# Kernel optimization log

Measured on AMD Instinct MI355X. Metric: run time of the kernel, lower is better.

Reference implementation:

```python
import jax, jax.numpy as jnp
import numpy as np

B, N, G = 4096, 20, 4
D_IN, D_OUT, H = 128, 64, 8
LRELU = 0.2  # TF leaky_relu default alpha


def _glorot(key, shape):
    fan_in, fan_out = shape[-2], shape[-1]
    scale = jnp.sqrt(6.0 / (fan_in + fan_out)).astype(jnp.float32)
    return jax.random.uniform(key, shape, jnp.float32, -1.0, 1.0) * scale


def setup_inputs() -> dict:
    key = jax.random.key(0)
    k1, k2, k3, k4, k5, k6 = jax.random.split(key, 6)
    return {
        "self_vecs": jax.random.normal(k1, (B, G, D_IN), jnp.float32),
        "neigh_vecs": jax.random.normal(k2, (B, N, G, D_IN), jnp.float32),
        "W_heads": _glorot(k3, (H, D_IN, D_OUT)),      # per-head before_attend_weights
        "a_self": _glorot(k4, (H, D_OUT, 1))[..., 0],  # per-head attend_weights_self  [H, D_OUT]
        "a_neigh": _glorot(k5, (H, D_OUT, 1))[..., 0], # per-head attend_weights_neigh [H, D_OUT]
        "W_out": _glorot(k6, (H * D_OUT, D_OUT)),      # final FC weights
    }


def reference(self_vecs, neigh_vecs, W_heads, a_self, a_neigh, W_out):
    # Transform self and neighbor vectors for all heads at once.
    self_t = jnp.einsum("bgd,hde->bghe", self_vecs, W_heads)    # [B,G,H,E]
    neigh_t = jnp.einsum("bngd,hde->bnghe", neigh_vecs, W_heads)  # [B,N,G,H,E]

    f_self = jnp.einsum("bghe,he->bgh", self_t, a_self)          # [B,G,H]
    f_neigh = jnp.einsum("bnghe,he->bngh", neigh_t, a_neigh)     # [B,N,G,H]

    # logits [B,N,G,H]; original applies softmax over the num_graphs axis (tf default last axis of [B,N,G])
    logits = f_self[:, None, :, :] + f_neigh
    attend = jax.nn.softmax(jax.nn.leaky_relu(logits, LRELU), axis=2)  # softmax over G

    # Weighted aggregation over neighbors: [B,G,H,E]
    out_h = jnp.einsum("bngh,bnghe->bghe", attend, neigh_t)
    out_h = jax.nn.leaky_relu(out_h, LRELU)  # per-head activation (act=leaky_relu)

    # Concatenate heads along feature dim -> [B,G,H*E], final FC + relu
    h = out_h.reshape(out_h.shape[0], out_h.shape[1], H * D_OUT)
    return jax.nn.relu(jnp.einsum("bgk,ke->bge", h, W_out))
```

## Files before the change

kernel.cpp:

```cpp
#include <hip/hip_runtime.h>
#include <hip/hip_bf16.h>

#define BB 4096
#define NNB 20
#define GG 4
#define DIN 128
#define EE 64
#define HH 8

typedef short bf16x8 __attribute__((ext_vector_type(8)));
typedef float f32x4 __attribute__((ext_vector_type(4)));

__device__ __forceinline__ float lrelu_f(float x) { return x > 0.f ? x : 0.2f * x; }
__device__ __forceinline__ unsigned short f2bf(float f) {
  unsigned u = __float_as_uint(f);
  return (unsigned short)((u + 0x7fffu + ((u >> 16) & 1u)) >> 16);
}
__device__ __forceinline__ float bf2f(unsigned short s) {
  return __uint_as_float(((unsigned)s) << 16);
}

__global__ __launch_bounds__(256) void prep_kernel(
    const float* __restrict__ W_heads, const float* __restrict__ a_self,
    const float* __restrict__ a_neigh, const float* __restrict__ W_out,
    unsigned short* __restrict__ P1Whi, unsigned short* __restrict__ P1Wlo,
    unsigned short* __restrict__ WBhi, unsigned short* __restrict__ WBlo,
    unsigned short* __restrict__ WOhi, unsigned short* __restrict__ WOlo) {
  int id = blockIdx.x * 256 + threadIdx.x;
  if (id < 2048) {
    int j = id & 7, lane = (id >> 3) & 63, kb = id >> 9;
    int col = lane & 15, k = kb * 32 + (lane >> 4) * 8 + j;
    int h = col & 7;
    const float* a = (col < 8) ? a_neigh : a_self;
    const float* Wrow = W_heads + (h * DIN + k) * EE;
    float acc = 0.f;
    for (int e = 0; e < EE; ++e) acc = fmaf(Wrow[e], a[h * EE + e], acc);
    unsigned short hi = f2bf(acc);
    P1Whi[id] = hi;
    P1Wlo[id] = f2bf(acc - bf2f(hi));
  } else if (id < 2048 + 65536) {
    int rel = id - 2048;
    int j = rel & 7, l = (rel >> 3) & 63, kb = (rel >> 9) & 3, nt = (rel >> 11) & 3, h = rel >> 13;
    int d = kb * 32 + (l >> 4) * 8 + j;
    int e = nt * 16 + (l & 15);
    float w = W_heads[(h * DIN + d) * EE + e];
    unsigned short hi = f2bf(w);
    WBhi[rel] = hi;
    WBlo[rel] = f2bf(w - bf2f(hi));
  } else if (id < 2048 + 65536 + 32768) {
    int rel = id - 2048 - 65536;
    int j = rel & 7, l = (rel >> 3) & 63, kb = (rel >> 9) & 15, nt = rel >> 13;
    int k = kb * 32 + (l >> 4) * 8 + j;
    int n = nt * 16 + (l & 15);
    float w = W_out[k * EE + n];
    unsigned short hi = f2bf(w);
    WOhi[rel] = hi;
    WOlo[rel] = f2bf(w - bf2f(hi));
  }
}

__global__ __launch_bounds__(512, 4) void fused_kernel(
    const float* __restrict__ self_vecs, const float* __restrict__ neigh_vecs,
    const unsigned short* __restrict__ P1Whi, const unsigned short* __restrict__ P1Wlo,
    const unsigned short* __restrict__ WBhi, const unsigned short* __restrict__ WBlo,
    const unsigned short* __restrict__ WOhi, const unsigned short* __restrict__ WOlo,
    float* __restrict__ out) {
  __shared__ char smem[57344];
  char* aggb = smem;
  float* attw = (float*)(smem + 32768);
  char* hb = smem + 32768;

  const int t = threadIdx.x;
  const int w = t >> 6, lane = t & 63;
  const int m = lane & 15, kg = lane >> 4;
  const int bid = blockIdx.x;

#define LOAD_X(X, ptr)                                                         \
  {                                                                            \
    const float4* p_ = (const float4*)(ptr);                                   \
    _Pragma("unroll") for (int q = 0; q < 4; ++q) {                            \
      X[2 * q]     = p_[q * 8 + kg * 2];                                       \
      X[2 * q + 1] = p_[q * 8 + kg * 2 + 1];                                   \
    }                                                                          \
  }

#define PROC_TILE(X, cvec)                                                     \
  {                                                                            \
    _Pragma("unroll") for (int kb = 0; kb < 4; ++kb) {                         \
      float xv[8] = {X[2 * kb].x,     X[2 * kb].y,     X[2 * kb].z,            \
                     X[2 * kb].w,     X[2 * kb + 1].x, X[2 * kb + 1].y,        \
                     X[2 * kb + 1].z, X[2 * kb + 1].w};                        \
      bf16x8 xh;                                                               \
      _Pragma("unroll") for (int j = 0; j < 8; ++j) xh[j] = (short)f2bf(xv[j]); \
      bf16x8 wh = *(const bf16x8*)(smem + kb * 1024 + lane * 16);              \
      bf16x8 wl = *(const bf16x8*)(smem + 4096 + kb * 1024 + lane * 16);       \
      cvec = __builtin_amdgcn_mfma_f32_16x16x32_bf16(xh, wh, cvec, 0, 0, 0);   \
      cvec = __builtin_amdgcn_mfma_f32_16x16x32_bf16(xh, wl, cvec, 0, 0, 0);   \
    }                                                                          \
  }

#define P1_SOFTMAX(tile, cvec)                                                 \
  if (m < 8) {                                                                 \
    float l[4], mx = -1e30f;                                                   \
    _Pragma("unroll") for (int gg = 0; gg < 4; ++gg) {                         \
      float v = lrelu_f(fs[gg] + (cvec)[gg]);                                  \
      l[gg] = v;                                                               \
      mx = fmaxf(mx, v);                                                       \
    }                                                                          \
    float s = 0.f;                                                             \
    _Pragma("unroll") for (int gg = 0; gg < 4; ++gg) {                         \
      l[gg] = __expf(l[gg] - mx);                                              \
      s += l[gg];                                                              \
    }                                                                          \
    float inv = 1.f / s;                                                       \
    _Pragma("unroll") for (int gg = 0; gg < 4; ++gg)                           \
      attw[(tile) * 128 + (kg * 4 + gg) * 8 + m] = l[gg] * inv;                \
  }

  const int bl_m = m >> 2, g_m = m & 3;
  const float* base_n =
      neigh_vecs + ((size_t)(bid * 4 + bl_m) * NNB * GG + g_m) * DIN;

  float4 XS[8], XA[8], XB[8], XC[8];
  LOAD_X(XS, self_vecs + ((size_t)bid * 16 + m) * DIN)
  LOAD_X(XA, base_n + (size_t)w * (GG * DIN))

  {
    const float4* src = (t < 256) ? (const float4*)P1Whi : (const float4*)P1Wlo;
    ((float4*)smem)[t] = src[t & 255];
  }
  __syncthreads();

  f32x4 fs;
  {
    f32x4 c20 = {0.f, 0.f, 0.f, 0.f};
    PROC_TILE(XS, c20)
#pragma unroll
    for (int reg = 0; reg < 4; ++reg) fs[reg] = __shfl_xor(c20[reg], 8);
  }
  LOAD_X(XB, base_n + (size_t)(w + 8) * (GG * DIN))

  f32x4 cA = {0.f, 0.f, 0.f, 0.f}, cB = {0.f, 0.f, 0.f, 0.f};
  PROC_TILE(XA, cA)
  if (w < 4) LOAD_X(XC, base_n + (size_t)(w + 16) * (GG * DIN))
  PROC_TILE(XB, cB)
  if (w < 4) {
    f32x4 cC = {0.f, 0.f, 0.f, 0.f};
    PROC_TILE(XC, cC)
    P1_SOFTMAX(w + 16, cC)
  }
  P1_SOFTMAX(w, cA)
  P1_SOFTMAX(w + 8, cB)
  __syncthreads();

  {
    const int ih = lane >> 5;
    const int bg = 2 * w + ih;
    const int bl = w >> 1;
    const int g0 = (2 * w) & 3;
    const float* nb2 =
        neigh_vecs + ((size_t)(bid * 4 + bl) * NNB * GG + g0) * DIN;
    const int dl = 4 * (lane & 31);
    float acc[8][4];
#pragma unroll
    for (int h = 0; h < 8; ++h)
#pragma unroll
      for (int d = 0; d < 4; ++d) acc[h][d] = 0.f;
#pragma unroll
    for (int n = 0; n < NNB; ++n) {
      float4 x4 = *(const float4*)&nb2[(size_t)n * GG * DIN + 4 * lane];
      f32x4 a0 = *(const f32x4*)&attw[n * 128 + bg * 8];
      f32x4 a1 = *(const f32x4*)&attw[n * 128 + bg * 8 + 4];
#pragma unroll
      for (int h = 0; h < 4; ++h) {
        acc[h][0] = fmaf(a0[h], x4.x, acc[h][0]);
        acc[h][1] = fmaf(a0[h], x4.y, acc[h][1]);
        acc[h][2] = fmaf(a0[h], x4.z, acc[h][2]);
        acc[h][3] = fmaf(a0[h], x4.w, acc[h][3]);
        acc[h + 4][0] = fmaf(a1[h], x4.x, acc[h + 4][0]);
        acc[h + 4][1] = fmaf(a1[h], x4.y, acc[h + 4][1]);
        acc[h + 4][2] = fmaf(a1[h], x4.z, acc[h + 4][2]);
        acc[h + 4][3] = fmaf(a1[h], x4.w, acc[h + 4][3]);
      }
    }
    const int swz = (bg & 7) << 4;
#pragma unroll
    for (int h = 0; h < 8; ++h) {
      uint2 pk;
      pk.x = (unsigned)f2bf(acc[h][0]) | ((unsigned)f2bf(acc[h][1]) << 16);
      pk.y = (unsigned)f2bf(acc[h][2]) | ((unsigned)f2bf(acc[h][3]) << 16);
      *(uint2*)(aggb + ((bg * 2048 + h * 256 + 2 * dl) ^ swz)) = pk;
    }
  }
  __syncthreads();

  {
    const int hh = w;
    const int aswz = (m & 7) << 4;
    bf16x8 a[4];
#pragma unroll
    for (int kb = 0; kb < 4; ++kb)
      a[kb] = *(const bf16x8*)(aggb + ((m * 2048 + hh * 256 + kb * 64 + kg * 16) ^ aswz));
#pragma unroll
    for (int nt = 0; nt < 4; ++nt) {
      f32x4 c = {0.f, 0.f, 0.f, 0.f};
#pragma unroll
      for (int kb = 0; kb < 4; ++kb) {
        const int fi = (((hh * 4 + nt) * 4 + kb) * 64 + lane) * 8;
        bf16x8 bh = *(const bf16x8*)(WBhi + fi);
        bf16x8 bl_ = *(const bf16x8*)(WBlo + fi);
        c = __builtin_amdgcn_mfma_f32_16x16x32_bf16(a[kb], bh, c, 0, 0, 0);
        c = __builtin_amdgcn_mfma_f32_16x16x32_bf16(a[kb], bl_, c, 0, 0, 0);
      }
      const int k = hh * 64 + nt * 16 + m;
#pragma unroll
      for (int reg = 0; reg < 4; ++reg) {
        int row = kg * 4 + reg;
        int byte = (row * 1024 + k * 2) ^ ((row & 7) << 4);
        *(unsigned short*)(hb + byte) = f2bf(lrelu_f(c[reg]));
      }
    }
  }
  __syncthreads();

  if (w < 4) {
    const int nt = w;
    f32x4 acc = {0.f, 0.f, 0.f, 0.f};
    for (int kb = 0; kb < 16; ++kb) {
      int byte = (m * 1024 + (kb * 32 + kg * 8) * 2) ^ ((m & 7) << 4);
      bf16x8 ah = *(const bf16x8*)(hb + byte);
      const int fi = ((nt * 16 + kb) * 64 + lane) * 8;
      bf16x8 bh = *(const bf16x8*)(WOhi + fi);
      bf16x8 bl_ = *(const bf16x8*)(WOlo + fi);
      acc = __builtin_amdgcn_mfma_f32_16x16x32_bf16(ah, bh, acc, 0, 0, 0);
      acc = __builtin_amdgcn_mfma_f32_16x16x32_bf16(ah, bl_, acc, 0, 0, 0);
    }
    const int rbase = bid * 16;
#pragma unroll
    for (int reg = 0; reg < 4; ++reg) {
      int row = rbase + kg * 4 + reg;
      out[(size_t)row * EE + nt * 16 + m] = fmaxf(acc[reg], 0.f);
    }
  }
#undef LOAD_X
#undef PROC_TILE
#undef P1_SOFTMAX
}

extern "C" void kernel_launch(void* const* d_in, const int* in_sizes, int n_in,
                              void* d_out, int out_size, void* d_ws, size_t ws_size,
                              hipStream_t stream) {
  (void)in_sizes; (void)n_in; (void)out_size; (void)ws_size;
  const float* self_vecs  = (const float*)d_in[0];
  const float* neigh_vecs = (const float*)d_in[1];
  const float* W_heads    = (const float*)d_in[2];
  const float* a_self     = (const float*)d_in[3];
  const float* a_neigh    = (const float*)d_in[4];
  const float* W_out      = (const float*)d_in[5];
  float* out              = (float*)d_out;

  char* ws = (char*)d_ws;
  unsigned short* P1Whi = (unsigned short*)ws;
  unsigned short* P1Wlo = (unsigned short*)(ws + 4096);
  unsigned short* WBhi  = (unsigned short*)(ws + 8192);
  unsigned short* WBlo  = (unsigned short*)(ws + 8192 + 131072);
  unsigned short* WOhi  = (unsigned short*)(ws + 8192 + 262144);
  unsigned short* WOlo  = (unsigned short*)(ws + 8192 + 262144 + 65536);

  prep_kernel<<<(2048 + 65536 + 32768) / 256, 256, 0, stream>>>(
      W_heads, a_self, a_neigh, W_out, P1Whi, P1Wlo, WBhi, WBlo, WOhi, WOlo);

  fused_kernel<<<BB / 4, 512, 0, stream>>>(
      self_vecs, neigh_vecs, P1Whi, P1Wlo, WBhi, WBlo, WOhi, WOlo, out);
}
```

Before: 68.07 us.

## Halve work per block: 2 batches per 256-thread block, 2048 blocks

Restructures the fused kernel so each block handles 2 batch items (8 rows) with 4 waves instead of 4 items with 8 waves, doubling the grid and cutting shared memory to 24KB. Phase-1 tiles are processed in a five-stage software pipeline with prefetching, and phases 2-3 loop over two heads per wave. MFMA tiles now run half-empty (rows duplicated via m&7), which wastes matrix throughput. In exchange the change aims for more blocks and better occupancy and latency hiding on the memory-bound neighbor reads.

```diff
diff --git a/kernel.cpp b/kernel.cpp
--- a/kernel.cpp
+++ b/kernel.cpp
@@ -59,20 +59,21 @@
   }
 }
 
-__global__ __launch_bounds__(512, 4) void fused_kernel(
+__global__ __launch_bounds__(256, 4) void fused_kernel(
     const float* __restrict__ self_vecs, const float* __restrict__ neigh_vecs,
     const unsigned short* __restrict__ P1Whi, const unsigned short* __restrict__ P1Wlo,
     const unsigned short* __restrict__ WBhi, const unsigned short* __restrict__ WBlo,
     const unsigned short* __restrict__ WOhi, const unsigned short* __restrict__ WOlo,
     float* __restrict__ out) {
-  __shared__ char smem[57344];
+  __shared__ char smem[24576];
   char* aggb = smem;
-  float* attw = (float*)(smem + 32768);
-  char* hb = smem + 32768;
+  float* attw = (float*)(smem + 16384);
+  char* hb = smem + 16384;
 
   const int t = threadIdx.x;
   const int w = t >> 6, lane = t & 63;
   const int m = lane & 15, kg = lane >> 4;
+  const int m8 = m & 7;
   const int bid = blockIdx.x;
 
 #define LOAD_X(X, ptr)                                                         \
@@ -100,7 +101,7 @@
   }
 
 #define P1_SOFTMAX(tile, cvec)                                                 \
-  if (m < 8) {                                                                 \
+  if (m < 8 && kg < 2) {                                                       \
     float l[4], mx = -1e30f;                                                   \
     _Pragma("unroll") for (int gg = 0; gg < 4; ++gg) {                         \
       float v = lrelu_f(fs[gg] + (cvec)[gg]);                                  \
@@ -114,21 +115,19 @@
     }                                                                          \
     float inv = 1.f / s;                                                       \
     _Pragma("unroll") for (int gg = 0; gg < 4; ++gg)                           \
-      attw[(tile) * 128 + (kg * 4 + gg) * 8 + m] = l[gg] * inv;                \
-  }
-
-  const int bl_m = m >> 2, g_m = m & 3;
+      attw[(tile) * 64 + (kg * 4 + gg) * 8 + m] = l[gg] * inv;                 \
+  }
+
+  const int bl8 = m8 >> 2, g8 = m8 & 3;
   const float* base_n =
-      neigh_vecs + ((size_t)(bid * 4 + bl_m) * NNB * GG + g_m) * DIN;
-
-  float4 XS[8], XA[8], XB[8], XC[8];
-  LOAD_X(XS, self_vecs + ((size_t)bid * 16 + m) * DIN)
+      neigh_vecs + (((size_t)(bid * 2 + bl8) * NNB) * GG + g8) * DIN;
+
+  float4 XS[8], XA[8], XB[8], XC[8], XD[8], XE[8];
+  LOAD_X(XS, self_vecs + ((size_t)bid * 8 + m8) * DIN)
   LOAD_X(XA, base_n + (size_t)w * (GG * DIN))
 
-  {
-    const float4* src = (t < 256) ? (const float4*)P1Whi : (const float4*)P1Wlo;
-    ((float4*)smem)[t] = src[t & 255];
-  }
+  ((float4*)smem)[t]       = ((const float4*)P1Whi)[t];
+  ((float4*)smem)[256 + t] = ((const float4*)P1Wlo)[t];
   __syncthreads();
 
   f32x4 fs;
@@ -138,28 +137,44 @@
 #pragma unroll
     for (int reg = 0; reg < 4; ++reg) fs[reg] = __shfl_xor(c20[reg], 8);
   }
-  LOAD_X(XB, base_n + (size_t)(w + 8) * (GG * DIN))
-
-  f32x4 cA = {0.f, 0.f, 0.f, 0.f}, cB = {0.f, 0.f, 0.f, 0.f};
-  PROC_TILE(XA, cA)
-  if (w < 4) LOAD_X(XC, base_n + (size_t)(w + 16) * (GG * DIN))
-  PROC_TILE(XB, cB)
-  if (w < 4) {
-    f32x4 cC = {0.f, 0.f, 0.f, 0.f};
-    PROC_TILE(XC, cC)
-    P1_SOFTMAX(w + 16, cC)
-  }
-  P1_SOFTMAX(w, cA)
-  P1_SOFTMAX(w + 8, cB)
+  LOAD_X(XB, base_n + (size_t)(w + 4) * (GG * DIN))
+
+  {
+    f32x4 c = {0.f, 0.f, 0.f, 0.f};
+    PROC_TILE(XA, c)
+    LOAD_X(XC, base_n + (size_t)(w + 8) * (GG * DIN))
+    P1_SOFTMAX(w, c)
+  }
+  {
+    f32x4 c = {0.f, 0.f, 0.f, 0.f};
+    PROC_TILE(XB, c)
+    LOAD_X(XD, base_n + (size_t)(w + 12) * (GG * DIN))
+    P1_SOFTMAX(w + 4, c)
+  }
+  {
+    f32x4 c = {0.f, 0.f, 0.f, 0.f};
+    PROC_TILE(XC, c)
+    LOAD_X(XE, base_n + (size_t)(w + 16) * (GG * DIN))
+    P1_SOFTMAX(w + 8, c)
+  }
+  {
+    f32x4 c = {0.f, 0.f, 0.f, 0.f};
+    PROC_TILE(XD, c)
+    P1_SOFTMAX(w + 12, c)
+  }
+  {
+    f32x4 c = {0.f, 0.f, 0.f, 0.f};
+    PROC_TILE(XE, c)
+    P1_SOFTMAX(w + 16, c)
+  }
   __syncthreads();
 
   {
     const int ih = lane >> 5;
     const int bg = 2 * w + ih;
-    const int bl = w >> 1;
     const int g0 = (2 * w) & 3;
     const float* nb2 =
-        neigh_vecs + ((size_t)(bid * 4 + bl) * NNB * GG + g0) * DIN;
+        neigh_vecs + (((size_t)(bid * 2 + (w >> 1)) * NNB) * GG + g0) * DIN;
     const int dl = 4 * (lane & 31);
     float acc[8][4];
 #pragma unroll
@@ -169,8 +184,8 @@
 #pragma unroll
     for (int n = 0; n < NNB; ++n) {
       float4 x4 = *(const float4*)&nb2[(size_t)n * GG * DIN + 4 * lane];
-      f32x4 a0 = *(const f32x4*)&attw[n * 128 + bg * 8];
-      f32x4 a1 = *(const f32x4*)&attw[n * 128 + bg * 8 + 4];
+      f32x4 a0 = *(const f32x4*)&attw[n * 64 + bg * 8];
+      f32x4 a1 = *(const f32x4*)&attw[n * 64 + bg * 8 + 4];
 #pragma unroll
       for (int h = 0; h < 4; ++h) {
         acc[h][0] = fmaf(a0[h], x4.x, acc[h][0]);
@@ -183,7 +198,7 @@
         acc[h + 4][3] = fmaf(a1[h], x4.w, acc[h + 4][3]);
       }
     }
-    const int swz = (bg & 7) << 4;
+    const int swz = bg << 4;
 #pragma unroll
     for (int h = 0; h < 8; ++h) {
       uint2 pk;
@@ -194,13 +209,14 @@
   }
   __syncthreads();
 
-  {
-    const int hh = w;
-    const int aswz = (m & 7) << 4;
+#pragma unroll
+  for (int hi_ = 0; hi_ < 2; ++hi_) {
+    const int hh = 2 * w + hi_;
+    const int aswz = m8 << 4;
     bf16x8 a[4];
 #pragma unroll
     for (int kb = 0; kb < 4; ++kb)
-      a[kb] = *(const bf16x8*)(aggb + ((m * 2048 + hh * 256 + kb * 64 + kg * 16) ^ aswz));
+      a[kb] = *(const bf16x8*)(aggb + ((m8 * 2048 + hh * 256 + kb * 64 + kg * 16) ^ aswz));
 #pragma unroll
     for (int nt = 0; nt < 4; ++nt) {
       f32x4 c = {0.f, 0.f, 0.f, 0.f};
@@ -212,22 +228,24 @@
         c = __builtin_amdgcn_mfma_f32_16x16x32_bf16(a[kb], bh, c, 0, 0, 0);
         c = __builtin_amdgcn_mfma_f32_16x16x32_bf16(a[kb], bl_, c, 0, 0, 0);
       }
-      const int k = hh * 64 + nt * 16 + m;
-#pragma unroll
-      for (int reg = 0; reg < 4; ++reg) {
-        int row = kg * 4 + reg;
-        int byte = (row * 1024 + k * 2) ^ ((row & 7) << 4);
-        *(unsigned short*)(hb + byte) = f2bf(lrelu_f(c[reg]));
-      }
-    }
-  }
-  __syncthreads();
-
-  if (w < 4) {
+      if (kg < 2) {
+        const int k = hh * 64 + nt * 16 + m;
+#pragma unroll
+        for (int reg = 0; reg < 4; ++reg) {
+          int row = kg * 4 + reg;
+          int byte = (row * 1024 + k * 2) ^ (row << 4);
+          *(unsigned short*)(hb + byte) = f2bf(lrelu_f(c[reg]));
+        }
+      }
+    }
+  }
+  __syncthreads();
+
+  {
     const int nt = w;
     f32x4 acc = {0.f, 0.f, 0.f, 0.f};
     for (int kb = 0; kb < 16; ++kb) {
-      int byte = (m * 1024 + (kb * 32 + kg * 8) * 2) ^ ((m & 7) << 4);
+      int byte = (m8 * 1024 + (kb * 32 + kg * 8) * 2) ^ (m8 << 4);
       bf16x8 ah = *(const bf16x8*)(hb + byte);
       const int fi = ((nt * 16 + kb) * 64 + lane) * 8;
       bf16x8 bh = *(const bf16x8*)(WOhi + fi);
@@ -235,11 +253,13 @@
       acc = __builtin_amdgcn_mfma_f32_16x16x32_bf16(ah, bh, acc, 0, 0, 0);
       acc = __builtin_amdgcn_mfma_f32_16x16x32_bf16(ah, bl_, acc, 0, 0, 0);
     }
-    const int rbase = bid * 16;
-#pragma unroll
-    for (int reg = 0; reg < 4; ++reg) {
-      int row = rbase + kg * 4 + reg;
-      out[(size_t)row * EE + nt * 16 + m] = fmaxf(acc[reg], 0.f);
+    if (kg < 2) {
+      const size_t rbase = (size_t)bid * 8;
+#pragma unroll
+      for (int reg = 0; reg < 4; ++reg) {
+        int row = kg * 4 + reg;
+        out[(rbase + row) * EE + nt * 16 + m] = fmaxf(acc[reg], 0.f);
+      }
     }
   }
 #undef LOAD_X
@@ -270,6 +290,6 @@
   prep_kernel<<<(2048 + 65536 + 32768) / 256, 256, 0, stream>>>(
       W_heads, a_self, a_neigh, W_out, P1Whi, P1Wlo, WBhi, WBlo, WOhi, WOlo);
 
-  fused_kernel<<<BB / 4, 512, 0, stream>>>(
+  fused_kernel<<<BB / 2, 256, 0, stream>>>(
       self_vecs, neigh_vecs, P1Whi, P1Wlo, WBhi, WBlo, WOhi, WOlo, out);
 }
```

Result: slower. 88.19 us (+29.6%).
